# Performance work log

Hardware: AMD Instinct MI355X
Metric: run time of the kernel (lower is better)

Reference implementation:

```python
import jax, jax.numpy as jnp
import numpy as np

N = 2048
INPUT_DIM = 256
OUTPUT_DIM = 512
NUM_HEADS = 8
HEAD_DIM = OUTPUT_DIM // NUM_HEADS


def _lin_init(key, fan_in, fan_out):
    # torch nn.Linear default init: U(-1/sqrt(fan_in), 1/sqrt(fan_in))
    kw, kb = jax.random.split(key)
    bound = 1.0 / np.sqrt(fan_in)
    W = jax.random.uniform(kw, (fan_in, fan_out), jnp.float32, -bound, bound)
    b = jax.random.uniform(kb, (fan_out,), jnp.float32, -bound, bound)
    return W, b


def setup_inputs() -> dict:
    key = jax.random.key(0)
    ks = jax.random.split(key, 12)
    x = jax.random.normal(ks[0], (N, INPUT_DIM), jnp.float32)
    rel_pos = jax.random.normal(ks[1], (N, 2), jnp.float32)
    rel_vel = jax.random.normal(ks[2], (N, 1), jnp.float32)
    rel_angle = jax.random.normal(ks[3], (N, 1), jnp.float32)
    Wq, bq = _lin_init(ks[4], INPUT_DIM, OUTPUT_DIM)
    Wk, bk = _lin_init(ks[5], INPUT_DIM, OUTPUT_DIM)
    Wv, bv = _lin_init(ks[6], INPUT_DIM, OUTPUT_DIM)
    Wsb1, bsb1 = _lin_init(ks[7], 2, HEAD_DIM)
    Wsb2, bsb2 = _lin_init(ks[8], HEAD_DIM, 1)
    Wmg1, bmg1 = _lin_init(ks[9], 2, HEAD_DIM)
    Wmg2, bmg2 = _lin_init(ks[10], HEAD_DIM, 1)
    Wo, bo = _lin_init(ks[11], OUTPUT_DIM, 1)
    return dict(x=x, rel_pos=rel_pos, rel_vel=rel_vel, rel_angle=rel_angle,
                Wq=Wq, bq=bq, Wk=Wk, bk=bk, Wv=Wv, bv=bv,
                Wsb1=Wsb1, bsb1=bsb1, Wsb2=Wsb2, bsb2=bsb2,
                Wmg1=Wmg1, bmg1=bmg1, Wmg2=Wmg2, bmg2=bmg2,
                Wo=Wo, bo=bo)


def reference(x, rel_pos, rel_vel, rel_angle,
              Wq, bq, Wk, bk, Wv, bv,
              Wsb1, bsb1, Wsb2, bsb2,
              Wmg1, bmg1, Wmg2, bmg2,
              Wo, bo):
    n = x.shape[0]
    Q = (x @ Wq + bq).reshape(n, NUM_HEADS, HEAD_DIM)
    K = (x @ Wk + bk).reshape(n, NUM_HEADS, HEAD_DIM)
    V = (x @ Wv + bv).reshape(n, NUM_HEADS, HEAD_DIM)

    # scores[q, k, h] = <Q[q,h], K[k,h]> / sqrt(head_dim)
    scores = jnp.einsum('qhd,khd->qkh', Q, K) / np.sqrt(HEAD_DIM).astype(np.float32)

    # spatial bias: per-query scalar, broadcast over keys and heads
    sb = (jax.nn.relu(rel_pos @ Wsb1 + bsb1) @ Wsb2 + bsb2)  # (N, 1)
    scores = scores + sb[:, :, None]  # (N,1,1) broadcast -> (N,N,H)

    # softmax over key dim (dim=1)
    attention = jax.nn.softmax(scores, axis=1)

    # motion gate: per-key scalar in (0,1)
    motion_feat = jnp.concatenate([rel_vel, rel_angle], axis=-1)  # (N, 2)
    mg = jax.nn.sigmoid(jax.nn.relu(motion_feat @ Wmg1 + bmg1) @ Wmg2 + bmg2)  # (N, 1)
    attention = attention * mg[None, :, 0, None]  # (1,N,1) broadcast

    # weighted sum over keys without materializing (N,N,H,D)
    out = jnp.einsum('qkh,khd->qhd', attention, V).reshape(n, OUTPUT_DIM)
    out = out @ Wo + bo  # (N, 1)
    return out[:, 0]
```

## Files before the change

### kernel.cpp

```cpp
#include <hip/hip_runtime.h>
#include <hip/hip_bf16.h>

constexpr int N    = 2048;
constexpr int IN   = 256;
constexpr int OUT  = 512;
constexpr int NH   = 8;
constexpr int HD   = 64;
constexpr int NQK  = 1024;
constexpr int NC   = 16;
constexpr int KPB  = N / NC;
constexpr int KT   = KPB / 16;

typedef _Float16  f16x8  __attribute__((ext_vector_type(8)));
typedef _Float16  f16x4  __attribute__((ext_vector_type(4)));
typedef float     f32x4  __attribute__((ext_vector_type(4)));

#if __has_builtin(__builtin_amdgcn_exp2f)
#define EXP2(x) __builtin_amdgcn_exp2f(x)
#else
#define EXP2(x) exp2f(x)
#endif

#define QSCALE (0.125f * 1.44269504088896f)

__global__ __launch_bounds__(256)
void prep_all(const float* __restrict__ x,
              const float* __restrict__ Wq, const float* __restrict__ Wk,
              const float* __restrict__ Wv, const float* __restrict__ bv,
              const float* __restrict__ Wo,
              _Float16* __restrict__ X16, _Float16* __restrict__ WT,
              float* __restrict__ Wvo, float* __restrict__ bvo) {
    __shared__ float smem[32 * 33];
    const int b = blockIdx.x;
    const int tid = threadIdx.x;

    if (b < 512) {
        const size_t i4 = ((size_t)b * 256 + tid) * 4;
        const float4 v = *(const float4*)(x + i4);
        f16x4 o;
        o[0] = (_Float16)v.x; o[1] = (_Float16)v.y;
        o[2] = (_Float16)v.z; o[3] = (_Float16)v.w;
        *(f16x4*)(X16 + i4) = o;
    } else if (b < 768) {
        const int tb = b - 512;
        const int k0 = (tb & 7) * 32;
        const int n0 = (tb >> 3) * 32;
        const float* W = (n0 < OUT) ? Wq : Wk;
        const int nc = (n0 < OUT) ? n0 : n0 - OUT;
        {
            const int row = tid >> 3;
            const int c4  = (tid & 7) * 4;
            const float4 v = *(const float4*)(W + (size_t)(k0 + row) * OUT + nc + c4);
            smem[row * 33 + c4 + 0] = v.x;
            smem[row * 33 + c4 + 1] = v.y;
            smem[row * 33 + c4 + 2] = v.z;
            smem[row * 33 + c4 + 3] = v.w;
        }
        __syncthreads();
        {
            const int nrow = tid >> 3;
            const int k4   = (tid & 7) * 4;
            f16x4 o;
            #pragma unroll
            for (int j = 0; j < 4; j++)
                o[j] = (_Float16)smem[(k4 + j) * 33 + nrow];
            *(f16x4*)(WT + (size_t)(n0 + nrow) * IN + k0 + k4) = o;
        }
    } else {
        float* wo_s = smem;
        wo_s[tid]       = Wo[tid];
        wo_s[tid + 256] = Wo[tid + 256];
        __syncthreads();
        const int i = (b - 768) * 32 + (tid >> 3);
        const int h = tid & 7;
        const float* wr = Wv + (size_t)i * OUT + h * HD;
        float s = 0.f;
        #pragma unroll
        for (int d = 0; d < HD; d += 4) {
            const float4 v = *(const float4*)(wr + d);
            s += v.x * wo_s[h * HD + d + 0] + v.y * wo_s[h * HD + d + 1]
               + v.z * wo_s[h * HD + d + 2] + v.w * wo_s[h * HD + d + 3];
        }
        Wvo[i * NH + h] = s;
        if (b == 768 && tid < NH) {
            float sb = 0.f;
            #pragma unroll
            for (int d = 0; d < HD; d++)
                sb += bv[tid * HD + d] * wo_s[tid * HD + d];
            bvo[tid] = sb;
        }
    }
}

__global__ __launch_bounds__(256)
void gemm_qk_vpm(const _Float16* __restrict__ X16, const _Float16* __restrict__ WT,
                 const float* __restrict__ bq, const float* __restrict__ bk,
                 _Float16* __restrict__ Qh, _Float16* __restrict__ Kh,
                 const float* __restrict__ x, const float* __restrict__ rel_vel,
                 const float* __restrict__ rel_angle,
                 const float* __restrict__ Wmg1, const float* __restrict__ bmg1,
                 const float* __restrict__ Wmg2, const float* __restrict__ bmg2,
                 const float* __restrict__ Wvo, const float* __restrict__ bvo,
                 float* __restrict__ vpmT) {
    __shared__ _Float16 stage[32 * 132];
    __shared__ float wvo_s[IN * NH];
    const int tid = threadIdx.x;

    if (blockIdx.x >= 512) {
        #pragma unroll
        for (int i = 0; i < 8; i++) wvo_s[tid + 256 * i] = Wvo[tid + 256 * i];
        __syncthreads();

        const int k = (blockIdx.x - 512) * 32 + (tid >> 3);
        const int h = tid & 7;

        const float m0 = rel_vel[k], m1 = rel_angle[k];
        float g = bmg2[0];
        #pragma unroll
        for (int j = 0; j < HD; j++) {
            float t = m0 * Wmg1[j] + m1 * Wmg1[HD + j] + bmg1[j];
            t = fmaxf(t, 0.f);
            g += t * Wmg2[j];
        }
        const float mg = 1.f / (1.f + __expf(-g));

        const float4* xr = (const float4*)(x + (size_t)k * IN);
        float a0 = 0.f, a1 = 0.f, a2 = 0.f, a3 = 0.f;
        #pragma unroll 4
        for (int i = 0; i < IN / 4; i++) {
            const float4 v = xr[i];
            a0 += v.x * wvo_s[(i * 4 + 0) * NH + h];
            a1 += v.y * wvo_s[(i * 4 + 1) * NH + h];
            a2 += v.z * wvo_s[(i * 4 + 2) * NH + h];
            a3 += v.w * wvo_s[(i * 4 + 3) * NH + h];
        }
        vpmT[h * N + k] = mg * (a0 + a1 + a2 + a3 + bvo[h]);
        return;
    }

    const int lane = tid & 63;
    const int wave = tid >> 6;
    const int row16 = lane & 15;
    const int quad  = lane >> 4;
    const int nb0 = (blockIdx.x & 7) * 128;
    const int mb  = (blockIdx.x >> 3) * 32;
    const int nb  = nb0 + wave * 32;

    const size_t ar[2] = {(size_t)(mb + row16) * IN, (size_t)(mb + 16 + row16) * IN};
    const size_t br[2] = {(size_t)(nb + row16) * IN, (size_t)(nb + 16 + row16) * IN};

    f32x4 acc[2][2] = {};
    for (int k0 = 0; k0 < IN; k0 += 32) {
        const int ko = k0 + quad * 8;
        f16x8 a[2], bf[2];
        #pragma unroll
        for (int t = 0; t < 2; t++) {
            a[t]  = *(const f16x8*)(X16 + ar[t] + ko);
            bf[t] = *(const f16x8*)(WT + br[t] + ko);
        }
        #pragma unroll
        for (int mt = 0; mt < 2; mt++)
            #pragma unroll
            for (int nt = 0; nt < 2; nt++)
                acc[mt][nt] = __builtin_amdgcn_mfma_f32_16x16x32_f16(a[mt], bf[nt], acc[mt][nt], 0, 0, 0);
    }

    const bool isQ = (nb0 < OUT);
    const float scale = isQ ? QSCALE : 1.0f;
    #pragma unroll
    for (int mt = 0; mt < 2; mt++)
        #pragma unroll
        for (int nt = 0; nt < 2; nt++) {
            const int nl = wave * 32 + nt * 16 + row16;
            const int np = nb0 + nl;
            const int nq = isQ ? np : np - OUT;
            const float bias = isQ ? bq[nq] : bk[nq];
            #pragma unroll
            for (int r = 0; r < 4; r++) {
                const int ml = mt * 16 + quad * 4 + r;
                stage[ml * 132 + nl] = (_Float16)((acc[mt][nt][r] + bias) * scale);
            }
        }
    __syncthreads();

    _Float16* dst = isQ ? Qh : Kh;
    const int r2   = tid >> 2;
    const int cidx = tid & 3;
    const int hl   = r2 >> 5;
    const int m    = r2 & 31;
    const int nqh  = (isQ ? nb0 : nb0 - OUT) + hl * 64;
    const int h    = nqh >> 6;
    const size_t goff = ((size_t)h * N + mb + m) * HD + cidx * 16;
    const int soff = m * 132 + hl * 64 + cidx * 16;
    *(f16x8*)(dst + goff)     = *(const f16x8*)(&stage[soff]);
    *(f16x8*)(dst + goff + 8) = *(const f16x8*)(&stage[soff + 8]);
}

__global__ __launch_bounds__(256)
void attn_mfma(const _Float16* __restrict__ Qh, const _Float16* __restrict__ Kh,
               const float* __restrict__ vpmT,
               float* __restrict__ pnum, float* __restrict__ pden) {
    const int b = blockIdx.x;
    const int h = b & 7;
    const int r = b >> 3;
    const int c = r >> 3;
    const int qg = r & 7;
    const int lane = threadIdx.x & 63;
    const int wave = threadIdx.x >> 6;
    const int q0 = (qg * 4 + wave) * 64;
    const int row16 = lane & 15;
    const int quad  = lane >> 4;

    f16x8 Bq[4][2];
    #pragma unroll
    for (int qt = 0; qt < 4; qt++) {
        const size_t qoff = ((size_t)h * N + q0 + qt * 16 + row16) * HD + quad * 8;
        Bq[qt][0] = *(const f16x8*)(Qh + qoff);
        Bq[qt][1] = *(const f16x8*)(Qh + qoff + 32);
    }

    float num[4] = {}, den[4] = {};
    const int k0 = c * KPB;
    const size_t kbase = ((size_t)h * N + k0 + row16) * HD + quad * 8;
    const float* vp = vpmT + h * N + k0 + quad * 4;

    f16x8 A0 = *(const f16x8*)(Kh + kbase);
    f16x8 A1 = *(const f16x8*)(Kh + kbase + 32);
    f32x4 vv = *(const f32x4*)(vp);

    #pragma unroll
    for (int t = 0; t < KT; t++) {
        const int tn = (t + 1 < KT) ? t + 1 : t;
        const size_t ka = kbase + (size_t)tn * 16 * HD;
        const f16x8 nA0 = *(const f16x8*)(Kh + ka);
        const f16x8 nA1 = *(const f16x8*)(Kh + ka + 32);
        const f32x4 nvv = *(const f32x4*)(vp + tn * 16);

        #pragma unroll
        for (int qt = 0; qt < 4; qt++) {
            f32x4 s = {0.f, 0.f, 0.f, 0.f};
            s = __builtin_amdgcn_mfma_f32_16x16x32_f16(A0, Bq[qt][0], s, 0, 0, 0);
            s = __builtin_amdgcn_mfma_f32_16x16x32_f16(A1, Bq[qt][1], s, 0, 0, 0);
            #pragma unroll
            for (int r4 = 0; r4 < 4; r4++) {
                const float e = EXP2(s[r4]);
                num[qt] += e * vv[r4];
                den[qt] += e;
            }
        }
        A0 = nA0; A1 = nA1; vv = nvv;
    }

    #pragma unroll
    for (int qt = 0; qt < 4; qt++) {
        float n = num[qt], d = den[qt];
        n += __shfl_xor(n, 16, 64);  d += __shfl_xor(d, 16, 64);
        n += __shfl_xor(n, 32, 64);  d += __shfl_xor(d, 32, 64);
        if (quad == 0) {
            const int q = q0 + qt * 16 + row16;
            pnum[((size_t)c * NH + h) * N + q] = n;
            pden[((size_t)c * NH + h) * N + q] = d;
        }
    }
}

__global__ __launch_bounds__(256)
void finalize(const float* __restrict__ pnum, const float* __restrict__ pden,
              const float* __restrict__ bo, float* __restrict__ out) {
    const int q = blockIdx.x * 256 + threadIdx.x;
    float acc = bo[0];
    #pragma unroll
    for (int h = 0; h < NH; h++) {
        float num = 0.f, den = 0.f;
        #pragma unroll
        for (int ci = 0; ci < NC; ci++) {
            num += pnum[((size_t)ci * NH + h) * N + q];
            den += pden[((size_t)ci * NH + h) * N + q];
        }
        acc += num / den;
    }
    out[q] = acc;
}

extern "C" void kernel_launch(void* const* d_in, const int* in_sizes, int n_in,
                              void* d_out, int out_size, void* d_ws, size_t ws_size,
                              hipStream_t stream) {
    const float* x         = (const float*)d_in[0];
    const float* rel_vel   = (const float*)d_in[2];
    const float* rel_angle = (const float*)d_in[3];
    const float* Wq        = (const float*)d_in[4];
    const float* bq        = (const float*)d_in[5];
    const float* Wk        = (const float*)d_in[6];
    const float* bk        = (const float*)d_in[7];
    const float* Wv        = (const float*)d_in[8];
    const float* bv        = (const float*)d_in[9];
    const float* Wmg1      = (const float*)d_in[14];
    const float* bmg1      = (const float*)d_in[15];
    const float* Wmg2      = (const float*)d_in[16];
    const float* bmg2      = (const float*)d_in[17];
    const float* Wo        = (const float*)d_in[18];
    const float* bo        = (const float*)d_in[19];
    float* out = (float*)d_out;

    _Float16* X16 = (_Float16*)d_ws;
    _Float16* WT  = X16 + (size_t)N * IN;
    _Float16* Qh  = WT + (size_t)NQK * IN;
    _Float16* Kh  = Qh + (size_t)NH * N * HD;
    float* fp     = (float*)(Kh + (size_t)NH * N * HD);
    float* Wvo    = fp;
    float* bvo    = Wvo + IN * NH;
    float* vpmT   = bvo + NH;
    float* pnum   = vpmT + NH * N;
    float* pden   = pnum + (size_t)NC * NH * N;

    hipLaunchKernelGGL(prep_all, dim3(776), dim3(256), 0, stream,
                       x, Wq, Wk, Wv, bv, Wo, X16, WT, Wvo, bvo);
    hipLaunchKernelGGL(gemm_qk_vpm, dim3(576), dim3(256), 0, stream,
                       X16, WT, bq, bk, Qh, Kh,
                       x, rel_vel, rel_angle, Wmg1, bmg1, Wmg2, bmg2, Wvo, bvo, vpmT);
    hipLaunchKernelGGL(attn_mfma, dim3(1024), dim3(256), 0, stream,
                       Qh, Kh, vpmT, pnum, pden);
    hipLaunchKernelGGL(finalize, dim3(8), dim3(256), 0, stream, pnum, pden, bo, out);
}
```

Measured before the change: 134.7 us.

## Fuse prep into QK GEMM and finalize into attention via atomic counters

Drops the separate prep kernel. The QK GEMM now loads fp32 x and Wq/Wk directly and converts them to fp16 in registers, and each vpm block recomputes Wv·Wo into shared memory itself. The finalize kernel becomes a last-block-done reduction inside the attention kernel, using per-query-group atomic counters that the first kernel resets. This cuts the launch count from four to two, but adds strided uncoalesced weight loads, redundant Wvo computation in 64 blocks, and atomic/fence overhead.

Measured after the change: 175.2 us. +30.0%, slower.

```diff
diff --git a/kernel.cpp b/kernel.cpp
--- a/kernel.cpp
+++ b/kernel.cpp
@@ -6,13 +6,11 @@
 constexpr int OUT  = 512;
 constexpr int NH   = 8;
 constexpr int HD   = 64;
-constexpr int NQK  = 1024;
 constexpr int NC   = 16;
 constexpr int KPB  = N / NC;
 constexpr int KT   = KPB / 16;
 
 typedef _Float16  f16x8  __attribute__((ext_vector_type(8)));
-typedef _Float16  f16x4  __attribute__((ext_vector_type(4)));
 typedef float     f32x4  __attribute__((ext_vector_type(4)));
 
 #if __has_builtin(__builtin_amdgcn_exp2f)
@@ -24,91 +22,51 @@
 #define QSCALE (0.125f * 1.44269504088896f)
 
 __global__ __launch_bounds__(256)
-void prep_all(const float* __restrict__ x,
-              const float* __restrict__ Wq, const float* __restrict__ Wk,
-              const float* __restrict__ Wv, const float* __restrict__ bv,
-              const float* __restrict__ Wo,
-              _Float16* __restrict__ X16, _Float16* __restrict__ WT,
-              float* __restrict__ Wvo, float* __restrict__ bvo) {
-    __shared__ float smem[32 * 33];
-    const int b = blockIdx.x;
+void fused_qk_vpm(const float* __restrict__ x,
+                  const float* __restrict__ Wq, const float* __restrict__ bq,
+                  const float* __restrict__ Wk, const float* __restrict__ bk,
+                  const float* __restrict__ Wv, const float* __restrict__ bv,
+                  const float* __restrict__ Wo,
+                  const float* __restrict__ rel_vel, const float* __restrict__ rel_angle,
+                  const float* __restrict__ Wmg1, const float* __restrict__ bmg1,
+                  const float* __restrict__ Wmg2, const float* __restrict__ bmg2,
+                  _Float16* __restrict__ Qh, _Float16* __restrict__ Kh,
+                  float* __restrict__ vpmT,
+                  unsigned* __restrict__ counters) {
+    __shared__ float smem[2568];
     const int tid = threadIdx.x;
 
-    if (b < 512) {
-        const size_t i4 = ((size_t)b * 256 + tid) * 4;
-        const float4 v = *(const float4*)(x + i4);
-        f16x4 o;
-        o[0] = (_Float16)v.x; o[1] = (_Float16)v.y;
-        o[2] = (_Float16)v.z; o[3] = (_Float16)v.w;
-        *(f16x4*)(X16 + i4) = o;
-    } else if (b < 768) {
-        const int tb = b - 512;
-        const int k0 = (tb & 7) * 32;
-        const int n0 = (tb >> 3) * 32;
-        const float* W = (n0 < OUT) ? Wq : Wk;
-        const int nc = (n0 < OUT) ? n0 : n0 - OUT;
-        {
-            const int row = tid >> 3;
-            const int c4  = (tid & 7) * 4;
-            const float4 v = *(const float4*)(W + (size_t)(k0 + row) * OUT + nc + c4);
-            smem[row * 33 + c4 + 0] = v.x;
-            smem[row * 33 + c4 + 1] = v.y;
-            smem[row * 33 + c4 + 2] = v.z;
-            smem[row * 33 + c4 + 3] = v.w;
-        }
-        __syncthreads();
-        {
-            const int nrow = tid >> 3;
-            const int k4   = (tid & 7) * 4;
-            f16x4 o;
-            #pragma unroll
-            for (int j = 0; j < 4; j++)
-                o[j] = (_Float16)smem[(k4 + j) * 33 + nrow];
-            *(f16x4*)(WT + (size_t)(n0 + nrow) * IN + k0 + k4) = o;
-        }
-    } else {
-        float* wo_s = smem;
+    if (blockIdx.x >= 512) {
+        float* wo_s  = smem;
+        float* wvo_s = smem + 512;
+        float* bvo_s = smem + 2560;
         wo_s[tid]       = Wo[tid];
         wo_s[tid + 256] = Wo[tid + 256];
+        if (blockIdx.x == 512 && tid < 8) counters[tid] = 0u;
         __syncthreads();
-        const int i = (b - 768) * 32 + (tid >> 3);
-        const int h = tid & 7;
-        const float* wr = Wv + (size_t)i * OUT + h * HD;
-        float s = 0.f;
-        #pragma unroll
-        for (int d = 0; d < HD; d += 4) {
-            const float4 v = *(const float4*)(wr + d);
-            s += v.x * wo_s[h * HD + d + 0] + v.y * wo_s[h * HD + d + 1]
-               + v.z * wo_s[h * HD + d + 2] + v.w * wo_s[h * HD + d + 3];
-        }
-        Wvo[i * NH + h] = s;
-        if (b == 768 && tid < NH) {
+
+        #pragma unroll
+        for (int rep = 0; rep < 8; rep++) {
+            const int idx = rep * 256 + tid;
+            const int i = idx >> 3, h = idx & 7;
+            const float* wr = Wv + (size_t)i * OUT + h * HD;
+            const float* wo = wo_s + h * HD;
+            float s = 0.f;
+            #pragma unroll
+            for (int d = 0; d < HD; d += 4) {
+                const float4 v = *(const float4*)(wr + d);
+                s += v.x * wo[d + 0] + v.y * wo[d + 1]
+                   + v.z * wo[d + 2] + v.w * wo[d + 3];
+            }
+            wvo_s[i * NH + h] = s;
+        }
+        if (tid < NH) {
+            const float* wo = wo_s + tid * HD;
             float sb = 0.f;
             #pragma unroll
-            for (int d = 0; d < HD; d++)
-                sb += bv[tid * HD + d] * wo_s[tid * HD + d];
-            bvo[tid] = sb;
-        }
-    }
-}
-
-__global__ __launch_bounds__(256)
-void gemm_qk_vpm(const _Float16* __restrict__ X16, const _Float16* __restrict__ WT,
-                 const float* __restrict__ bq, const float* __restrict__ bk,
-                 _Float16* __restrict__ Qh, _Float16* __restrict__ Kh,
-                 const float* __restrict__ x, const float* __restrict__ rel_vel,
-                 const float* __restrict__ rel_angle,
-                 const float* __restrict__ Wmg1, const float* __restrict__ bmg1,
-                 const float* __restrict__ Wmg2, const float* __restrict__ bmg2,
-                 const float* __restrict__ Wvo, const float* __restrict__ bvo,
-                 float* __restrict__ vpmT) {
-    __shared__ _Float16 stage[32 * 132];
-    __shared__ float wvo_s[IN * NH];
-    const int tid = threadIdx.x;
-
-    if (blockIdx.x >= 512) {
-        #pragma unroll
-        for (int i = 0; i < 8; i++) wvo_s[tid + 256 * i] = Wvo[tid + 256 * i];
+            for (int d = 0; d < HD; d++) sb += bv[tid * HD + d] * wo[d];
+            bvo_s[tid] = sb;
+        }
         __syncthreads();
 
         const int k = (blockIdx.x - 512) * 32 + (tid >> 3);
@@ -134,29 +92,48 @@
             a2 += v.z * wvo_s[(i * 4 + 2) * NH + h];
             a3 += v.w * wvo_s[(i * 4 + 3) * NH + h];
         }
-        vpmT[h * N + k] = mg * (a0 + a1 + a2 + a3 + bvo[h]);
+        vpmT[h * N + k] = mg * (a0 + a1 + a2 + a3 + bvo_s[h]);
         return;
     }
 
-    const int lane = tid & 63;
-    const int wave = tid >> 6;
+    const int lane  = tid & 63;
+    const int wave  = tid >> 6;
     const int row16 = lane & 15;
     const int quad  = lane >> 4;
     const int nb0 = (blockIdx.x & 7) * 128;
     const int mb  = (blockIdx.x >> 3) * 32;
-    const int nb  = nb0 + wave * 32;
-
-    const size_t ar[2] = {(size_t)(mb + row16) * IN, (size_t)(mb + 16 + row16) * IN};
-    const size_t br[2] = {(size_t)(nb + row16) * IN, (size_t)(nb + 16 + row16) * IN};
+    const bool isQ = (nb0 < OUT);
+    const float* Wsel = isQ ? Wq : Wk;
+    const int ncb = (isQ ? nb0 : nb0 - OUT) + wave * 32 + row16;
+
+    const float* xr0 = x + (size_t)(mb + row16) * IN;
+    const float* xr1 = x + (size_t)(mb + 16 + row16) * IN;
 
     f32x4 acc[2][2] = {};
     for (int k0 = 0; k0 < IN; k0 += 32) {
         const int ko = k0 + quad * 8;
         f16x8 a[2], bf[2];
-        #pragma unroll
-        for (int t = 0; t < 2; t++) {
-            a[t]  = *(const f16x8*)(X16 + ar[t] + ko);
-            bf[t] = *(const f16x8*)(WT + br[t] + ko);
+        {
+            const float4 u0 = *(const float4*)(xr0 + ko);
+            const float4 u1 = *(const float4*)(xr0 + ko + 4);
+            a[0][0] = (_Float16)u0.x; a[0][1] = (_Float16)u0.y;
+            a[0][2] = (_Float16)u0.z; a[0][3] = (_Float16)u0.w;
+            a[0][4] = (_Float16)u1.x; a[0][5] = (_Float16)u1.y;
+            a[0][6] = (_Float16)u1.z; a[0][7] = (_Float16)u1.w;
+            const float4 v0 = *(const float4*)(xr1 + ko);
+            const float4 v1 = *(const float4*)(xr1 + ko + 4);
+            a[1][0] = (_Float16)v0.x; a[1][1] = (_Float16)v0.y;
+            a[1][2] = (_Float16)v0.z; a[1][3] = (_Float16)v0.w;
+            a[1][4] = (_Float16)v1.x; a[1][5] = (_Float16)v1.y;
+            a[1][6] = (_Float16)v1.z; a[1][7] = (_Float16)v1.w;
+        }
+        #pragma unroll
+        for (int nt = 0; nt < 2; nt++) {
+            const float* wp = Wsel + (size_t)ko * OUT + ncb + nt * 16;
+            f16x8 b;
+            #pragma unroll
+            for (int j = 0; j < 8; j++) b[j] = (_Float16)wp[(size_t)j * OUT];
+            bf[nt] = b;
         }
         #pragma unroll
         for (int mt = 0; mt < 2; mt++)
@@ -165,7 +142,7 @@
                 acc[mt][nt] = __builtin_amdgcn_mfma_f32_16x16x32_f16(a[mt], bf[nt], acc[mt][nt], 0, 0, 0);
     }
 
-    const bool isQ = (nb0 < OUT);
+    _Float16* stage = (_Float16*)smem;
     const float scale = isQ ? QSCALE : 1.0f;
     #pragma unroll
     for (int mt = 0; mt < 2; mt++)
@@ -197,9 +174,10 @@
 }
 
 __global__ __launch_bounds__(256)
-void attn_mfma(const _Float16* __restrict__ Qh, const _Float16* __restrict__ Kh,
-               const float* __restrict__ vpmT,
-               float* __restrict__ pnum, float* __restrict__ pden) {
+void attn_fin(const _Float16* __restrict__ Qh, const _Float16* __restrict__ Kh,
+              const float* __restrict__ vpmT, const float* __restrict__ bo,
+              float* __restrict__ pnum, float* __restrict__ pden,
+              unsigned* __restrict__ counters, float* __restrict__ out) {
     const int b = blockIdx.x;
     const int h = b & 7;
     const int r = b >> 3;
@@ -262,24 +240,30 @@
             pden[((size_t)c * NH + h) * N + q] = d;
         }
     }
-}
-
-__global__ __launch_bounds__(256)
-void finalize(const float* __restrict__ pnum, const float* __restrict__ pden,
-              const float* __restrict__ bo, float* __restrict__ out) {
-    const int q = blockIdx.x * 256 + threadIdx.x;
-    float acc = bo[0];
-    #pragma unroll
-    for (int h = 0; h < NH; h++) {
-        float num = 0.f, den = 0.f;
-        #pragma unroll
-        for (int ci = 0; ci < NC; ci++) {
-            num += pnum[((size_t)ci * NH + h) * N + q];
-            den += pden[((size_t)ci * NH + h) * N + q];
-        }
-        acc += num / den;
-    }
-    out[q] = acc;
+
+    __syncthreads();
+    __shared__ int last;
+    if (threadIdx.x == 0) {
+        __threadfence();
+        last = (atomicAdd(&counters[qg], 1u) == (unsigned)(NC * NH - 1));
+    }
+    __syncthreads();
+    if (last) {
+        __threadfence();
+        const int q = qg * 256 + (int)threadIdx.x;
+        float acc = bo[0];
+        #pragma unroll
+        for (int hh = 0; hh < NH; hh++) {
+            float n = 0.f, d = 0.f;
+            #pragma unroll
+            for (int ci = 0; ci < NC; ci++) {
+                n += pnum[((size_t)ci * NH + hh) * N + q];
+                d += pden[((size_t)ci * NH + hh) * N + q];
+            }
+            acc += n / d;
+        }
+        out[q] = acc;
+    }
 }
 
 extern "C" void kernel_launch(void* const* d_in, const int* in_sizes, int n_in,
@@ -302,23 +286,17 @@
     const float* bo        = (const float*)d_in[19];
     float* out = (float*)d_out;
 
-    _Float16* X16 = (_Float16*)d_ws;
-    _Float16* WT  = X16 + (size_t)N * IN;
-    _Float16* Qh  = WT + (size_t)NQK * IN;
-    _Float16* Kh  = Qh + (size_t)NH * N * HD;
-    float* fp     = (float*)(Kh + (size_t)NH * N * HD);
-    float* Wvo    = fp;
-    float* bvo    = Wvo + IN * NH;
-    float* vpmT   = bvo + NH;
-    float* pnum   = vpmT + NH * N;
-    float* pden   = pnum + (size_t)NC * NH * N;
-
-    hipLaunchKernelGGL(prep_all, dim3(776), dim3(256), 0, stream,
-                       x, Wq, Wk, Wv, bv, Wo, X16, WT, Wvo, bvo);
-    hipLaunchKernelGGL(gemm_qk_vpm, dim3(576), dim3(256), 0, stream,
-                       X16, WT, bq, bk, Qh, Kh,
-                       x, rel_vel, rel_angle, Wmg1, bmg1, Wmg2, bmg2, Wvo, bvo, vpmT);
-    hipLaunchKernelGGL(attn_mfma, dim3(1024), dim3(256), 0, stream,
-                       Qh, Kh, vpmT, pnum, pden);
-    hipLaunchKernelGGL(finalize, dim3(8), dim3(256), 0, stream, pnum, pden, bo, out);
+    _Float16* Qh   = (_Float16*)d_ws;
+    _Float16* Kh   = Qh + (size_t)NH * N * HD;
+    float* vpmT    = (float*)(Kh + (size_t)NH * N * HD);
+    float* pnum    = vpmT + (size_t)NH * N;
+    float* pden    = pnum + (size_t)NC * NH * N;
+    unsigned* counters = (unsigned*)(pden + (size_t)NC * NH * N);
+
+    hipLaunchKernelGGL(fused_qk_vpm, dim3(576), dim3(256), 0, stream,
+                       x, Wq, bq, Wk, bk, Wv, bv, Wo,
+                       rel_vel, rel_angle, Wmg1, bmg1, Wmg2, bmg2,
+                       Qh, Kh, vpmT, counters);
+    hipLaunchKernelGGL(attn_fin, dim3(1024), dim3(256), 0, stream,
+                       Qh, Kh, vpmT, bo, pnum, pden, counters, out);
 }
```
